# Kernel tuning notes

Hardware: AMD Instinct MI355X
Metric: run time of the kernel (lower is better)

Reference implementation:

```python
import jax, jax.numpy as jnp
import numpy as np

N, C_IN, C_OUT = 8192, 256, 128


def setup_inputs() -> dict:
    key = jax.random.key(0)
    k1, k2, k3, k4, k5 = jax.random.split(key, 5)
    features = jax.random.normal(k1, (N, C_IN), dtype=jnp.float32)
    wavelets = jax.random.normal(k2, (N, N), dtype=jnp.float32) / np.sqrt(N)
    wavelets_inv = jax.random.normal(k3, (N, N), dtype=jnp.float32) / np.sqrt(N)
    # xavier_uniform for weight_matrix
    limit = np.sqrt(6.0 / (C_IN + C_OUT))
    weight_matrix = jax.random.uniform(k4, (C_IN, C_OUT), dtype=jnp.float32, minval=-limit, maxval=limit)
    # filter init uniform(0.9, 1.1)
    filt = jax.random.uniform(k5, (N,), dtype=jnp.float32, minval=0.9, maxval=1.1)
    return {"features": features, "wavelets": wavelets, "wavelets_inv": wavelets_inv,
            "weight_matrix": weight_matrix, "filt": filt}


def reference(features, wavelets, wavelets_inv, weight_matrix, filt):
    # transformed = features @ W                         [N, C_out]
    transformed = jnp.matmul(features, weight_matrix)
    # right = wavelets_inv @ transformed                 [N, C_out]
    right = jnp.matmul(wavelets_inv, transformed)
    # wavelets @ diag(filt) == column-wise scale of wavelets by filt
    # (same math as torch.mm(wavelets, torch.diag(filter)) without the O(N^3) GEMM)
    scaled_right = right * filt[:, None]                 # equivalent: (wavelets * filt) @ right
    out = jnp.matmul(wavelets, scaled_right)             # [N, C_out]
    return out
```

## Files before the change

### kernel.cpp

```cpp
#include <hip/hip_runtime.h>

#define MROWS 8192
#define NCOLS 128
#define KSTEP 128
#define BM    16
#define LDT   136

using f32x4  = __attribute__((ext_vector_type(4))) float;
using bf16x8 = __attribute__((ext_vector_type(8))) short;
using u32x4  = __attribute__((ext_vector_type(4))) unsigned int;
using u32x2  = __attribute__((ext_vector_type(2))) unsigned int;

__device__ __forceinline__ unsigned short f2bf(float f) {
    unsigned int u = __float_as_uint(f);
    u += 0x7fffu + ((u >> 16) & 1u);
    return (unsigned short)(u >> 16);
}
__device__ __forceinline__ unsigned int pk2(float a, float b) {
    return (unsigned int)f2bf(a) | ((unsigned int)f2bf(b) << 16);
}

template <int OUTMODE>
__global__ __launch_bounds__(256, 2) void gemm_tall(
    const float* __restrict__ A,
    const unsigned short* __restrict__ Bt,
    void* __restrict__ out,
    const float* __restrict__ filt,
    int Kdim, int ldb)
{
    __shared__ __align__(16) unsigned short As[BM * LDT];
    __shared__ __align__(16) unsigned short Bs[128 * LDT];

    const int tid  = threadIdx.x;
    const int lane = tid & 63;
    const int wn   = (tid >> 6) * 32;
    const int lrow = lane & 15;
    const int lq   = lane >> 4;
    const int m0   = blockIdx.x * BM;

    const int arow = tid >> 4;
    const int ak   = (tid & 15) * 8;
    const int brow = tid >> 1;
    const int bk   = (tid & 1) * 64;

    const float*          Ap = A  + (size_t)(m0 + arow) * Kdim + ak;
    const unsigned short* Bp = Bt + (size_t)brow * ldb + bk;

    f32x4 a0[2], a1[2];
    u32x4 b0[8], b1[8];

#define LDG(a, b, k0) do { \
        a[0] = *(const f32x4*)(Ap + (k0));              \
        a[1] = *(const f32x4*)(Ap + (k0) + 4);          \
        const unsigned short* bp_ = Bp + (k0);          \
        _Pragma("unroll")                               \
        for (int i_ = 0; i_ < 8; ++i_)                  \
            b[i_] = *(const u32x4*)(bp_ + i_ * 8);      \
    } while (0)

#define STG(a, b) do { \
        u32x4 av_;                                      \
        av_.x = pk2(a[0].x, a[0].y);                    \
        av_.y = pk2(a[0].z, a[0].w);                    \
        av_.z = pk2(a[1].x, a[1].y);                    \
        av_.w = pk2(a[1].z, a[1].w);                    \
        *(u32x4*)&As[arow * LDT + ak] = av_;            \
        _Pragma("unroll")                               \
        for (int i_ = 0; i_ < 8; ++i_)                  \
            *(u32x4*)&Bs[brow * LDT + bk + i_ * 8] = b[i_]; \
    } while (0)

    f32x4 acc0 = {0.f, 0.f, 0.f, 0.f};
    f32x4 acc1 = {0.f, 0.f, 0.f, 0.f};

    auto COMPUTE = [&]() {
#pragma unroll
        for (int kk = 0; kk < 4; ++kk) {
            const int ko = kk * 32 + lq * 8;
            bf16x8 af  = *(bf16x8*)&As[lrow * LDT + ko];
            bf16x8 bf0 = *(bf16x8*)&Bs[(wn + lrow) * LDT + ko];
            bf16x8 bf1 = *(bf16x8*)&Bs[(wn + 16 + lrow) * LDT + ko];
            acc0 = __builtin_amdgcn_mfma_f32_16x16x32_bf16(af, bf0, acc0, 0, 0, 0);
            acc1 = __builtin_amdgcn_mfma_f32_16x16x32_bf16(af, bf1, acc1, 0, 0, 0);
        }
    };

    const int iters = Kdim / KSTEP;
    LDG(a0, b0, 0);
    LDG(a1, b1, KSTEP);
    STG(a0, b0);
    __syncthreads();

    for (int it = 0; it < iters; it += 2) {
        if (it + 2 < iters) LDG(a0, b0, (it + 2) * KSTEP);
        COMPUTE();
        __syncthreads();
        STG(a1, b1);
        __syncthreads();
        if (it + 3 < iters) LDG(a1, b1, (it + 3) * KSTEP);
        COMPUTE();
        if (it + 2 < iters) {
            __syncthreads();
            STG(a0, b0);
            __syncthreads();
        }
    }
#undef LDG
#undef STG

    const int r = m0 + lq * 4;
    if (OUTMODE == 2) {
        float* O = (float*)out;
#pragma unroll
        for (int nt = 0; nt < 2; ++nt) {
            const int c = wn + nt * 16 + lrow;
            const f32x4 v = nt ? acc1 : acc0;
#pragma unroll
            for (int e = 0; e < 4; ++e)
                O[(size_t)(r + e) * NCOLS + c] = v[e];
        }
    } else {
        unsigned short* O = (unsigned short*)out;
        f32x4 v0 = acc0, v1 = acc1;
        if (OUTMODE == 1) {
            const f32x4 fl = *(const f32x4*)&filt[r];
            v0 *= fl;
            v1 *= fl;
        }
        u32x2 o;
        o.x = pk2(v0.x, v0.y); o.y = pk2(v0.z, v0.w);
        *(u32x2*)&O[(size_t)(wn + lrow) * MROWS + r] = o;
        o.x = pk2(v1.x, v1.y); o.y = pk2(v1.z, v1.w);
        *(u32x2*)&O[(size_t)(wn + 16 + lrow) * MROWS + r] = o;
    }
}

__global__ void convert_w(const float* __restrict__ W, unsigned short* __restrict__ Wt) {
    int idx = blockIdx.x * 256 + threadIdx.x;
    int k = idx >> 7, c = idx & 127;
    Wt[c * 256 + k] = f2bf(W[idx]);
}

extern "C" void kernel_launch(void* const* d_in, const int* in_sizes, int n_in,
                              void* d_out, int out_size, void* d_ws, size_t ws_size,
                              hipStream_t stream) {
    const float* features     = (const float*)d_in[0];
    const float* wavelets     = (const float*)d_in[1];
    const float* wavelets_inv = (const float*)d_in[2];
    const float* W            = (const float*)d_in[3];
    const float* filt         = (const float*)d_in[4];
    float* outp = (float*)d_out;

    char* ws = (char*)d_ws;
    unsigned short* Tt = (unsigned short*)ws;
    unsigned short* Rt = (unsigned short*)(ws + (size_t)2 * 1024 * 1024);
    unsigned short* Wt = (unsigned short*)(ws + (size_t)4 * 1024 * 1024);

    convert_w<<<128, 256, 0, stream>>>(W, Wt);
    gemm_tall<0><<<512, 256, 0, stream>>>(features,     Wt, (void*)Tt,   nullptr, 256,  256);
    gemm_tall<1><<<512, 256, 0, stream>>>(wavelets_inv, Tt, (void*)Rt,   filt,    8192, 8192);
    gemm_tall<2><<<512, 256, 0, stream>>>(wavelets,     Rt, (void*)outp, nullptr, 8192, 8192);
}
```

Baseline: 685.6 us.

## Stream GEMM operands straight into registers with an XCD-aware tile mapping

```diff
diff --git a/kernel.cpp b/kernel.cpp
--- a/kernel.cpp
+++ b/kernel.cpp
@@ -2,9 +2,6 @@
 
 #define MROWS 8192
 #define NCOLS 128
-#define KSTEP 128
-#define BM    16
-#define LDT   136
 
 using f32x4  = __attribute__((ext_vector_type(4))) float;
 using bf16x8 = __attribute__((ext_vector_type(8))) short;
@@ -19,101 +16,98 @@
 __device__ __forceinline__ unsigned int pk2(float a, float b) {
     return (unsigned int)f2bf(a) | ((unsigned int)f2bf(b) << 16);
 }
+__device__ __forceinline__ bf16x8 cvt8(f32x4 lo, f32x4 hi) {
+    union { u32x4 u; bf16x8 h; } r;
+    r.u.x = pk2(lo.x, lo.y); r.u.y = pk2(lo.z, lo.w);
+    r.u.z = pk2(hi.x, hi.y); r.u.w = pk2(hi.z, hi.w);
+    return r.h;
+}
+__device__ __forceinline__ bf16x8 asbf(u32x4 v) {
+    union { u32x4 u; bf16x8 h; } r; r.u = v; return r.h;
+}
+
+struct Buf {
+    f32x4 a[2][2];
+    u32x4 b[2][2];
+};
 
 template <int OUTMODE>
-__global__ __launch_bounds__(256, 2) void gemm_tall(
+__global__ __launch_bounds__(256) void gemm_stream(
     const float* __restrict__ A,
     const unsigned short* __restrict__ Bt,
     void* __restrict__ out,
     const float* __restrict__ filt,
     int Kdim, int ldb)
 {
-    __shared__ __align__(16) unsigned short As[BM * LDT];
-    __shared__ __align__(16) unsigned short Bs[128 * LDT];
-
     const int tid  = threadIdx.x;
     const int lane = tid & 63;
-    const int wn   = (tid >> 6) * 32;
+    const int wv   = tid >> 6;
+    const int wm   = (wv >> 1) * 16;
+    const int wn   = (wv & 1) * 32;
     const int lrow = lane & 15;
     const int lq   = lane >> 4;
-    const int m0   = blockIdx.x * BM;
 
-    const int arow = tid >> 4;
-    const int ak   = (tid & 15) * 8;
-    const int brow = tid >> 1;
-    const int bk   = (tid & 1) * 64;
+    const int bid   = blockIdx.x;
+    const int xcd   = bid & 7;
+    const int slot  = bid >> 3;
+    const int mtile = xcd * 32 + (slot >> 1);
+    const int nhalf = slot & 1;
 
-    const float*          Ap = A  + (size_t)(m0 + arow) * Kdim + ak;
-    const unsigned short* Bp = Bt + (size_t)brow * ldb + bk;
+    const int mbase = mtile * 32 + wm;
+    const int cbase = nhalf * 64 + wn;
 
-    f32x4 a0[2], a1[2];
-    u32x4 b0[8], b1[8];
-
-#define LDG(a, b, k0) do { \
-        a[0] = *(const f32x4*)(Ap + (k0));              \
-        a[1] = *(const f32x4*)(Ap + (k0) + 4);          \
-        const unsigned short* bp_ = Bp + (k0);          \
-        _Pragma("unroll")                               \
-        for (int i_ = 0; i_ < 8; ++i_)                  \
-            b[i_] = *(const u32x4*)(bp_ + i_ * 8);      \
-    } while (0)
-
-#define STG(a, b) do { \
-        u32x4 av_;                                      \
-        av_.x = pk2(a[0].x, a[0].y);                    \
-        av_.y = pk2(a[0].z, a[0].w);                    \
-        av_.z = pk2(a[1].x, a[1].y);                    \
-        av_.w = pk2(a[1].z, a[1].w);                    \
-        *(u32x4*)&As[arow * LDT + ak] = av_;            \
-        _Pragma("unroll")                               \
-        for (int i_ = 0; i_ < 8; ++i_)                  \
-            *(u32x4*)&Bs[brow * LDT + bk + i_ * 8] = b[i_]; \
-    } while (0)
+    const float*          Ap  = A  + (size_t)(mbase + lrow) * Kdim + lq * 8;
+    const unsigned short* Bp0 = Bt + (size_t)(cbase + lrow) * ldb + lq * 8;
+    const unsigned short* Bp1 = Bp0 + (size_t)16 * ldb;
 
     f32x4 acc0 = {0.f, 0.f, 0.f, 0.f};
     f32x4 acc1 = {0.f, 0.f, 0.f, 0.f};
 
-    auto COMPUTE = [&]() {
-#pragma unroll
-        for (int kk = 0; kk < 4; ++kk) {
-            const int ko = kk * 32 + lq * 8;
-            bf16x8 af  = *(bf16x8*)&As[lrow * LDT + ko];
-            bf16x8 bf0 = *(bf16x8*)&Bs[(wn + lrow) * LDT + ko];
-            bf16x8 bf1 = *(bf16x8*)&Bs[(wn + 16 + lrow) * LDT + ko];
-            acc0 = __builtin_amdgcn_mfma_f32_16x16x32_bf16(af, bf0, acc0, 0, 0, 0);
-            acc1 = __builtin_amdgcn_mfma_f32_16x16x32_bf16(af, bf1, acc1, 0, 0, 0);
-        }
-    };
+    Buf s0, s1, s2, s3;
 
-    const int iters = Kdim / KSTEP;
-    LDG(a0, b0, 0);
-    LDG(a1, b1, KSTEP);
-    STG(a0, b0);
-    __syncthreads();
+#define LOADB(B, ks) do { \
+        B.a[0][0] = *(const f32x4*)(Ap + (ks));          \
+        B.a[0][1] = *(const f32x4*)(Ap + (ks) + 4);      \
+        B.a[1][0] = *(const f32x4*)(Ap + (ks) + 32);     \
+        B.a[1][1] = *(const f32x4*)(Ap + (ks) + 36);     \
+        B.b[0][0] = *(const u32x4*)(Bp0 + (ks));         \
+        B.b[0][1] = *(const u32x4*)(Bp0 + (ks) + 32);    \
+        B.b[1][0] = *(const u32x4*)(Bp1 + (ks));         \
+        B.b[1][1] = *(const u32x4*)(Bp1 + (ks) + 32);    \
+    } while (0)
 
-    for (int it = 0; it < iters; it += 2) {
-        if (it + 2 < iters) LDG(a0, b0, (it + 2) * KSTEP);
-        COMPUTE();
-        __syncthreads();
-        STG(a1, b1);
-        __syncthreads();
-        if (it + 3 < iters) LDG(a1, b1, (it + 3) * KSTEP);
-        COMPUTE();
-        if (it + 2 < iters) {
-            __syncthreads();
-            STG(a0, b0);
-            __syncthreads();
-        }
+#define COMP(B) do { \
+        bf16x8 af0 = cvt8(B.a[0][0], B.a[0][1]);                                   \
+        acc0 = __builtin_amdgcn_mfma_f32_16x16x32_bf16(af0, asbf(B.b[0][0]), acc0, 0, 0, 0); \
+        acc1 = __builtin_amdgcn_mfma_f32_16x16x32_bf16(af0, asbf(B.b[1][0]), acc1, 0, 0, 0); \
+        bf16x8 af1 = cvt8(B.a[1][0], B.a[1][1]);                                   \
+        acc0 = __builtin_amdgcn_mfma_f32_16x16x32_bf16(af1, asbf(B.b[0][1]), acc0, 0, 0, 0); \
+        acc1 = __builtin_amdgcn_mfma_f32_16x16x32_bf16(af1, asbf(B.b[1][1]), acc1, 0, 0, 0); \
+    } while (0)
+
+    const int iters = Kdim >> 6;
+    LOADB(s0, 0);
+    LOADB(s1, 64);
+    for (int it = 0; it < iters; it += 4) {
+        const int ks = it * 64;
+        if (it + 2 < iters) LOADB(s2, ks + 128);
+        COMP(s0);
+        if (it + 3 < iters) LOADB(s3, ks + 192);
+        COMP(s1);
+        if (it + 4 < iters) LOADB(s0, ks + 256);
+        COMP(s2);
+        if (it + 5 < iters) LOADB(s1, ks + 320);
+        COMP(s3);
     }
-#undef LDG
-#undef STG
+#undef LOADB
+#undef COMP
 
-    const int r = m0 + lq * 4;
+    const int r = mbase + lq * 4;
     if (OUTMODE == 2) {
         float* O = (float*)out;
 #pragma unroll
         for (int nt = 0; nt < 2; ++nt) {
-            const int c = wn + nt * 16 + lrow;
+            const int c = cbase + nt * 16 + lrow;
             const f32x4 v = nt ? acc1 : acc0;
 #pragma unroll
             for (int e = 0; e < 4; ++e)
@@ -129,9 +123,9 @@
         }
         u32x2 o;
         o.x = pk2(v0.x, v0.y); o.y = pk2(v0.z, v0.w);
-        *(u32x2*)&O[(size_t)(wn + lrow) * MROWS + r] = o;
+        *(u32x2*)&O[(size_t)(cbase + lrow) * MROWS + r] = o;
         o.x = pk2(v1.x, v1.y); o.y = pk2(v1.z, v1.w);
-        *(u32x2*)&O[(size_t)(wn + 16 + lrow) * MROWS + r] = o;
+        *(u32x2*)&O[(size_t)(cbase + 16 + lrow) * MROWS + r] = o;
     }
 }
 
@@ -157,7 +151,7 @@
     unsigned short* Wt = (unsigned short*)(ws + (size_t)4 * 1024 * 1024);
 
     convert_w<<<128, 256, 0, stream>>>(W, Wt);
-    gemm_tall<0><<<512, 256, 0, stream>>>(features,     Wt, (void*)Tt,   nullptr, 256,  256);
-    gemm_tall<1><<<512, 256, 0, stream>>>(wavelets_inv, Tt, (void*)Rt,   filt,    8192, 8192);
-    gemm_tall<2><<<512, 256, 0, stream>>>(wavelets,     Rt, (void*)outp, nullptr, 8192, 8192);
+    gemm_stream<0><<<512, 256, 0, stream>>>(features,     Wt, (void*)Tt,   nullptr, 256,  256);
+    gemm_stream<1><<<512, 256, 0, stream>>>(wavelets_inv, Tt, (void*)Rt,   filt,    8192, 8192);
+    gemm_stream<2><<<512, 256, 0, stream>>>(wavelets,     Rt, (void*)outp, nullptr, 8192, 8192);
 }
```

Measured after the change: 839.6 us. 22.5% more time.
